# Performance work log

Hardware: AMD Instinct MI355X
Metric: run time of the kernel (lower is better)

Reference implementation:

```python
import jax, jax.numpy as jnp
import numpy as np

LNF, PNF, H = 128, 128, 128
THRESH = 10.0
NORM = 100.0
EPS = 1e-8


def _linear(x, W, b):
    return x @ W + b


def _glorot(key, shape):
    fan_in = shape[0]
    return jax.random.normal(key, shape, dtype=jnp.float32) / jnp.sqrt(jnp.float32(fan_in))


def setup_inputs() -> dict:
    key = jax.random.key(0)
    ks = jax.random.split(key, 20)
    bs, nl, npr = 4, 128, 1024
    inp = {
        "h_ligand": jax.random.normal(ks[0], (bs, nl, LNF), jnp.float32),
        "x_ligand": jax.random.normal(ks[1], (bs, nl, 3), jnp.float32) * 4.0,
        "h_protein": jax.random.normal(ks[2], (bs, npr, PNF), jnp.float32),
        "x_protein": jax.random.normal(ks[3], (bs, npr, 3), jnp.float32) * 4.0,
        "ligand_mask": jnp.ones((bs, nl, 1), jnp.float32),
        "protein_mask": jnp.ones((bs, npr, 1), jnp.float32),
        # attention MLP: (lnf+pnf+1)->H->H->1
        "aW1": _glorot(ks[4], (LNF + PNF + 1, H)), "ab1": jnp.zeros((H,), jnp.float32),
        "aW2": _glorot(ks[5], (H, H)),            "ab2": jnp.zeros((H,), jnp.float32),
        "aW3": _glorot(ks[6], (H, 1)),            "ab3": jnp.zeros((1,), jnp.float32),
        # value MLP: (pnf+1)->H->lnf
        "vW1": _glorot(ks[7], (PNF + 1, H)),      "vb1": jnp.zeros((H,), jnp.float32),
        "vW2": _glorot(ks[8], (H, LNF)),          "vb2": jnp.zeros((LNF,), jnp.float32),
        # coord MLP: (lnf+pnf+1)->H->1
        "cW1": _glorot(ks[9], (LNF + PNF + 1, H)), "cb1": jnp.zeros((H,), jnp.float32),
        "cW2": _glorot(ks[10], (H, 1)),           "cb2": jnp.zeros((1,), jnp.float32),
    }
    return inp


def reference(h_ligand, x_ligand, h_protein, x_protein, ligand_mask, protein_mask,
              aW1, ab1, aW2, ab2, aW3, ab3, vW1, vb1, vW2, vb2, cW1, cb1, cW2, cb2):
    bs, nl, lnf = h_ligand.shape
    npr = h_protein.shape[1]
    # pairwise geometry [bs, nl, np, ...]
    rel = x_ligand[:, :, None, :] - x_protein[:, None, :, :]
    ds = jnp.sum(rel * rel, axis=-1, keepdims=True)           # dist^2
    dist = jnp.sqrt(ds + EPS)
    edge = (dist < THRESH).astype(h_ligand.dtype)             # radius edge mask
    direction = rel / (dist + EPS)
    hl = jnp.broadcast_to(h_ligand[:, :, None, :], (bs, nl, npr, lnf))
    hp = jnp.broadcast_to(h_protein[:, None, :, :], (bs, nl, npr, h_protein.shape[-1]))
    pm = protein_mask[:, None, :, :]                          # [bs,1,np,1]

    pair_in = jnp.concatenate([hl, hp, ds], axis=-1)
    # attention MLP -> sigmoid
    a = jax.nn.silu(_linear(pair_in, aW1, ab1))
    a = jax.nn.silu(_linear(a, aW2, ab2))
    attn = jax.nn.sigmoid(_linear(a, aW3, ab3)) * pm
    # value MLP
    v = jax.nn.silu(_linear(jnp.concatenate([hp, ds], axis=-1), vW1, vb1))
    val = _linear(v, vW2, vb2)
    # feature messages, masked radius aggregation
    h_cross = jnp.sum(attn * val * edge, axis=2) / NORM       # [bs,nl,lnf]
    # coord MLP -> tanh
    c = jax.nn.silu(_linear(pair_in, cW1, cb1))
    cw = jnp.tanh(_linear(c, cW2, cb2)) * pm
    x_cross = jnp.sum(direction * cw * edge, axis=2) / NORM   # [bs,nl,3]

    h_cross = h_cross * ligand_mask
    x_cross = x_cross * ligand_mask
    return h_cross, x_cross
```

## Files before the change

kernel.cpp:

```cpp
#include <hip/hip_runtime.h>
#include <hip/hip_bf16.h>
#include <math.h>

#define HF 128
#define NL 128
#define NP 1024
#define NB 4
#define EPSF 1e-8f

typedef short bf16x8 __attribute__((ext_vector_type(8)));
typedef float f32x4 __attribute__((ext_vector_type(4)));

__device__ __forceinline__ float fast_rcp(float x){ return __builtin_amdgcn_rcpf(x); }
__device__ __forceinline__ float silu_f(float x){ return x*fast_rcp(1.f+__expf(-x)); }
__device__ __forceinline__ float sigmoid_f(float x){ return fast_rcp(1.f+__expf(-x)); }
__device__ __forceinline__ float tanh_f(float x){ return 1.f - 2.f*fast_rcp(1.f+__expf(2.f*x)); }
__device__ __forceinline__ unsigned short f2bf(float f){ __hip_bfloat16 h=__float2bfloat16(f); return *(unsigned short*)&h; }
__device__ __forceinline__ float bf2f(short u){ unsigned int x = ((unsigned int)(unsigned short)u)<<16; float r; __builtin_memcpy(&r,&x,4); return r; }

__global__ __launch_bounds__(128) void precompute_kernel(
    const float* __restrict__ h_ligand, const float* __restrict__ h_protein,
    const float* __restrict__ aW1, const float* __restrict__ ab1,
    const float* __restrict__ vW1, const float* __restrict__ vb1,
    const float* __restrict__ cW1, const float* __restrict__ cb1,
    const float* __restrict__ aW2, const float* __restrict__ vW2,
    float* __restrict__ Al, float* __restrict__ Cl,
    unsigned short* __restrict__ Ap, unsigned short* __restrict__ Vp,
    unsigned short* __restrict__ Cp,
    unsigned short* __restrict__ WaT, unsigned short* __restrict__ WvT)
{
    const int blk = blockIdx.x, n = threadIdx.x;
    if (blk < 64) {
        __shared__ float rows[8][HF];
        const int r0 = blk*8;
        for (int idx=n; idx<8*HF; idx+=128) rows[idx>>7][idx&127] = h_ligand[r0*HF+idx];
        __syncthreads();
        float aA[8], aC[8];
        const float bA = ab1[n], bC = cb1[n];
        #pragma unroll
        for (int r=0;r<8;++r){ aA[r]=bA; aC[r]=bC; }
        #pragma unroll 4
        for (int k=0;k<HF;++k){
            float wA = aW1[k*HF+n], wC = cW1[k*HF+n];
            #pragma unroll
            for (int r=0;r<8;++r){ aA[r]=fmaf(rows[r][k],wA,aA[r]); aC[r]=fmaf(rows[r][k],wC,aC[r]); }
        }
        #pragma unroll
        for (int r=0;r<8;++r){ Al[(r0+r)*HF+n]=aA[r]; Cl[(r0+r)*HF+n]=aC[r]; }
    } else if (blk < 576) {
        __shared__ float rows[8][HF];
        const int r0 = (blk-64)*8;
        for (int idx=n; idx<8*HF; idx+=128) rows[idx>>7][idx&127] = h_protein[r0*HF+idx];
        __syncthreads();
        float aA[8], aV[8], aC[8];
        const float bV = vb1[n];
        #pragma unroll
        for (int r=0;r<8;++r){ aA[r]=0.f; aV[r]=bV; aC[r]=0.f; }
        #pragma unroll 2
        for (int k=0;k<HF;++k){
            float wA = aW1[(HF+k)*HF+n], wV = vW1[k*HF+n], wC = cW1[(HF+k)*HF+n];
            #pragma unroll
            for (int r=0;r<8;++r){
                float h = rows[r][k];
                aA[r]=fmaf(h,wA,aA[r]); aV[r]=fmaf(h,wV,aV[r]); aC[r]=fmaf(h,wC,aC[r]);
            }
        }
        #pragma unroll
        for (int r=0;r<8;++r){
            Ap[(r0+r)*HF+n]=f2bf(aA[r]); Vp[(r0+r)*HF+n]=f2bf(aV[r]); Cp[(r0+r)*HF+n]=f2bf(aC[r]);
        }
    } else {
        const int m = blk - 576;
        const float* W = (m<8) ? aW2 : vW2;
        unsigned short* WT = (m<8) ? WaT : WvT;
        const int n0 = (m&7)*16;
        #pragma unroll
        for (int kb=0; kb<16; ++kb) {
            int k = kb*8 + (n>>4);
            int col = n0 + (n&15);
            WT[col*HF + k] = f2bf(W[k*HF + col]);
        }
    }
}

__global__ __launch_bounds__(256,2) void egnn_main_kernel(
    const float* __restrict__ x_ligand, const float* __restrict__ x_protein,
    const float* __restrict__ ligand_mask, const float* __restrict__ protein_mask,
    const float* __restrict__ aW1, const float* __restrict__ ab2,
    const float* __restrict__ aW3, const float* __restrict__ ab3,
    const float* __restrict__ vW1, const float* __restrict__ vb2,
    const float* __restrict__ cW1, const float* __restrict__ cW2, const float* __restrict__ cb2,
    const float* __restrict__ Al, const float* __restrict__ Cl,
    const unsigned short* __restrict__ Ap, const unsigned short* __restrict__ Vp,
    const unsigned short* __restrict__ Cp,
    const unsigned short* __restrict__ WaT, const unsigned short* __restrict__ WvT,
    float* __restrict__ out)
{
    __shared__ __align__(16) char smem[50176];
    float* ds_all = (float*)(smem + 32768);
    float* pme    = (float*)(smem + 34816);
    float* dirx   = (float*)(smem + 36864);
    float* diry   = (float*)(smem + 38912);
    float* dirz   = (float*)(smem + 40960);
    unsigned short* jlist = (unsigned short*)(smem + 43008);
    float* Al_s   = (float*)(smem + 44032);
    float* Cl_s   = (float*)(smem + 44544);
    float* aw1l   = (float*)(smem + 45056);
    float* cw1l   = (float*)(smem + 45568);
    float* vw1l   = (float*)(smem + 46080);
    float* cW2s   = (float*)(smem + 46592);
    float* attn_part = (float*)(smem + 47104);
    float* attn_e = (float*)(smem + 47360);
    float* hred   = (float*)(smem + 47616);
    float* xw     = (float*)(smem + 48640);
    int* nact_p   = (int*)(smem + 48704);

    const int t = threadIdx.x, lane = t&63, w = t>>6;
    const int wj = w>>1, wn = w&1;
    const int lr = lane&15, lg = lane>>4;
    const int bi = blockIdx.x;
    const int half = bi & 1;
    const int ii = bi >> 1;
    const int b = ii >> 7;
    const int jbase = half*512;

    const float xl0 = x_ligand[ii*3+0], xl1 = x_ligand[ii*3+1], xl2 = x_ligand[ii*3+2];
    const float* xp = x_protein + ((size_t)b*NP + jbase)*3;
    const float* pm = protein_mask + (size_t)b*NP + jbase;
    #pragma unroll
    for (int q=0; q<2; ++q) {
        int jj = q*256 + t;
        float r0 = xl0-xp[jj*3+0], r1 = xl1-xp[jj*3+1], r2 = xl2-xp[jj*3+2];
        float ds = r0*r0+r1*r1+r2*r2;
        float dist = sqrtf(ds+EPSF);
        float inv = fast_rcp(dist+EPSF);
        float e = dist < 10.f ? 1.f : 0.f;
        ds_all[jj]=ds; pme[jj]=pm[jj]*e;
        dirx[jj]=r0*inv; diry[jj]=r1*inv; dirz[jj]=r2*inv;
    }
    if (t < HF) {
        Al_s[t] = Al[(size_t)ii*HF+t];
        Cl_s[t] = Cl[(size_t)ii*HF+t];
        aw1l[t] = aW1[256*HF+t];
        cw1l[t] = cW1[256*HF+t];
        vw1l[t] = vW1[128*HF+t];
        cW2s[t] = cW2[t];
    }
    float ab2v[4], aw3v[4], vb2v[4];
    #pragma unroll
    for (int nt=0; nt<4; ++nt) {
        int n = wn*64 + nt*16 + lr;
        ab2v[nt] = ab2[n]; aw3v[nt] = aW3[n]; vb2v[nt] = vb2[n];
    }
    const float ab3v = ab3[0], cb2v = cb2[0];

    for (int c = t; c < 2048; c += 256) {
        int n = c >> 4, kc = c & 15;
        *(bf16x8*)(smem + n*256 + ((kc*16) ^ ((n&7)<<4))) = *(const bf16x8*)(WaT + n*HF + kc*8);
    }
    __syncthreads();

    if (w == 0) {
        int base = 0;
        for (int c=0; c<8; ++c) {
            int jj = c*64 + lane;
            bool act = pme[jj] > 0.f;
            unsigned long long m = __ballot(act);
            int pos = base + __popcll(m & ((1ull<<lane)-1ull));
            if (act) jlist[pos] = (unsigned short)jj;
            base += __popcll(m);
        }
        if (lane == 0) *nact_p = base;
    }
    bf16x8 wa[4][4], wv[4][4];
    #pragma unroll
    for (int nt = 0; nt < 4; ++nt) {
        int ncol = wn*64 + nt*16 + lr;
        int rb = ncol*256, sw = (ncol & 7) << 4;
        #pragma unroll
        for (int ks = 0; ks < 4; ++ks)
            wa[nt][ks] = *(bf16x8*)(smem + rb + ((lg*16 + ks*64) ^ sw));
    }
    __syncthreads();

    for (int c = t; c < 2048; c += 256) {
        int n = c >> 4, kc = c & 15;
        *(bf16x8*)(smem + n*256 + ((kc*16) ^ ((n&7)<<4))) = *(const bf16x8*)(WvT + n*HF + kc*8);
    }
    __syncthreads();
    #pragma unroll
    for (int nt = 0; nt < 4; ++nt) {
        int ncol = wn*64 + nt*16 + lr;
        int rb = ncol*256, sw = (ncol & 7) << 4;
        #pragma unroll
        for (int ks = 0; ks < 4; ++ks)
            wv[nt][ks] = *(bf16x8*)(smem + rb + ((lg*16 + ks*64) ^ sw));
    }
    __syncthreads();

    const int nact = *nact_p;
    const int ntiles = (nact + 31) >> 5;

    const unsigned short* Ap_b = Ap + ((size_t)b*NP + jbase)*HF;
    const unsigned short* Vp_b = Vp + ((size_t)b*NP + jbase)*HF;
    const unsigned short* Cp_b = Cp + ((size_t)b*NP + jbase)*HF;

    float hacc[4] = {0.f,0.f,0.f,0.f};
    float sae = 0.f;
    float xa0 = 0.f, xa1 = 0.f, xa2 = 0.f;
    const int brow = t >> 4, bcol = (t & 15)*8;
    const int crow = t >> 3, cg = t & 7;

    for (int tile = 0; tile < ntiles; ++tile) {
        const int j0 = tile*32;

        #pragma unroll
        for (int m = 0; m < 2; ++m) {
            const int row = m*16 + brow;
            const int grow = j0 + row;
            const int jl = jlist[grow < nact ? grow : 0];
            const float dsv = ds_all[jl];
            bf16x8 ap = *(const bf16x8*)(Ap_b + (size_t)jl*HF + bcol);
            f32x4 al0 = *(const f32x4*)&Al_s[bcol];
            f32x4 al1 = *(const f32x4*)&Al_s[bcol+4];
            f32x4 w0  = *(const f32x4*)&aw1l[bcol];
            f32x4 w1  = *(const f32x4*)&aw1l[bcol+4];
            bf16x8 pk;
            #pragma unroll
            for (int q = 0; q < 4; ++q) {
                pk[q]   = (short)f2bf(silu_f(al0[q] + bf2f(ap[q])   + dsv*w0[q]));
                pk[q+4] = (short)f2bf(silu_f(al1[q] + bf2f(ap[q+4]) + dsv*w1[q]));
            }
            *(bf16x8*)(smem + row*256 + ((bcol*2) ^ ((row & 7) << 4))) = pk;
        }
        __syncthreads();

        bf16x8 af[4];
        {
            int arow = wj*16 + lr;
            int rb = arow*256, sw = (arow & 7) << 4;
            #pragma unroll
            for (int ks = 0; ks < 4; ++ks)
                af[ks] = *(bf16x8*)(smem + rb + ((lg*16 + ks*64) ^ sw));
        }
        f32x4 acc[4];
        #pragma unroll
        for (int nt = 0; nt < 4; ++nt) {
            acc[nt] = (f32x4){0.f,0.f,0.f,0.f};
            #pragma unroll
            for (int ks = 0; ks < 4; ++ks)
                acc[nt] = __builtin_amdgcn_mfma_f32_16x16x32_bf16(af[ks], wa[nt][ks], acc[nt], 0,0,0);
        }
        {
            const int growc = j0 + crow;
            const bool okc = growc < nact;
            const int jlc = jlist[okc ? growc : 0];
            const float pmec = okc ? pme[jlc] : 0.f;
            const float dsc = ds_all[jlc];
            float part = 0.f;
            const unsigned short* cp = Cp_b + (size_t)jlc*HF + cg*16;
            #pragma unroll
            for (int u = 0; u < 2; ++u) {
                const int ch = cg*16 + u*8;
                bf16x8 cv = *(const bf16x8*)(cp + u*8);
                f32x4 cl0 = *(const f32x4*)&Cl_s[ch];
                f32x4 cl1 = *(const f32x4*)&Cl_s[ch+4];
                f32x4 w0  = *(const f32x4*)&cw1l[ch];
                f32x4 w1  = *(const f32x4*)&cw1l[ch+4];
                f32x4 s0  = *(const f32x4*)&cW2s[ch];
                f32x4 s1  = *(const f32x4*)&cW2s[ch+4];
                #pragma unroll
                for (int q = 0; q < 4; ++q) {
                    part += silu_f(cl0[q] + bf2f(cv[q])   + dsc*w0[q]) * s0[q];
                    part += silu_f(cl1[q] + bf2f(cv[q+4]) + dsc*w1[q]) * s1[q];
                }
            }
            part += __shfl_xor(part,1); part += __shfl_xor(part,2); part += __shfl_xor(part,4);
            if (cg == 0) {
                float cw = tanh_f(part + cb2v) * pmec;
                xa0 = fmaf(dirx[jlc], cw, xa0);
                xa1 = fmaf(diry[jlc], cw, xa1);
                xa2 = fmaf(dirz[jlc], cw, xa2);
            }
        }
        #pragma unroll
        for (int r = 0; r < 4; ++r) {
            float p = 0.f;
            #pragma unroll
            for (int nt = 0; nt < 4; ++nt)
                p += silu_f(acc[nt][r] + ab2v[nt]) * aw3v[nt];
            p += __shfl_xor(p,1); p += __shfl_xor(p,2);
            p += __shfl_xor(p,4); p += __shfl_xor(p,8);
            if (lr == 0) attn_part[wn*32 + wj*16 + lg*4 + r] = p;
        }
        __syncthreads();

        if (t < 32) {
            const int grow = j0 + t;
            const bool ok = grow < nact;
            const int j = jlist[ok ? grow : 0];
            attn_e[t] = sigmoid_f(attn_part[t] + attn_part[32+t] + ab3v) * (ok ? pme[j] : 0.f);
        }
        #pragma unroll
        for (int m = 0; m < 2; ++m) {
            const int row = m*16 + brow;
            const int grow = j0 + row;
            const int jl = jlist[grow < nact ? grow : 0];
            const float dsv = ds_all[jl];
            bf16x8 vp = *(const bf16x8*)(Vp_b + (size_t)jl*HF + bcol);
            f32x4 w0 = *(const f32x4*)&vw1l[bcol];
            f32x4 w1 = *(const f32x4*)&vw1l[bcol+4];
            bf16x8 pk;
            #pragma unroll
            for (int q = 0; q < 4; ++q) {
                pk[q]   = (short)f2bf(silu_f(bf2f(vp[q])   + dsv*w0[q]));
                pk[q+4] = (short)f2bf(silu_f(bf2f(vp[q+4]) + dsv*w1[q]));
            }
            *(bf16x8*)(smem + 8192 + row*256 + ((bcol*2) ^ ((row & 7) << 4))) = pk;
        }
        __syncthreads();

        bf16x8 vf[4];
        {
            int arow = wj*16 + lr;
            int rb = 8192 + arow*256, sw = (arow & 7) << 4;
            #pragma unroll
            for (int ks = 0; ks < 4; ++ks)
                vf[ks] = *(bf16x8*)(smem + rb + ((lg*16 + ks*64) ^ sw));
        }
        float ae[4];
        #pragma unroll
        for (int r = 0; r < 4; ++r) { ae[r] = attn_e[wj*16 + lg*4 + r]; sae += ae[r]; }
        #pragma unroll
        for (int nt = 0; nt < 4; ++nt) {
            f32x4 a = (f32x4){0.f,0.f,0.f,0.f};
            #pragma unroll
            for (int ks = 0; ks < 4; ++ks)
                a = __builtin_amdgcn_mfma_f32_16x16x32_bf16(vf[ks], wv[nt][ks], a, 0,0,0);
            hacc[nt] += ae[0]*a[0] + ae[1]*a[1] + ae[2]*a[2] + ae[3]*a[3];
        }
    }

    #pragma unroll
    for (int nt = 0; nt < 4; ++nt) {
        hacc[nt] += __shfl_xor(hacc[nt],16);
        hacc[nt] += __shfl_xor(hacc[nt],32);
    }
    sae += __shfl_xor(sae,16);
    sae += __shfl_xor(sae,32);
    if (lg == 0) {
        #pragma unroll
        for (int nt = 0; nt < 4; ++nt)
            hred[wj*128 + wn*64 + nt*16 + lr] = hacc[nt] + vb2v[nt]*sae;
    }
    xa0 += __shfl_xor(xa0,1);  xa1 += __shfl_xor(xa1,1);  xa2 += __shfl_xor(xa2,1);
    xa0 += __shfl_xor(xa0,2);  xa1 += __shfl_xor(xa1,2);  xa2 += __shfl_xor(xa2,2);
    xa0 += __shfl_xor(xa0,4);  xa1 += __shfl_xor(xa1,4);  xa2 += __shfl_xor(xa2,4);
    xa0 += __shfl_xor(xa0,8);  xa1 += __shfl_xor(xa1,8);  xa2 += __shfl_xor(xa2,8);
    xa0 += __shfl_xor(xa0,16); xa1 += __shfl_xor(xa1,16); xa2 += __shfl_xor(xa2,16);
    xa0 += __shfl_xor(xa0,32); xa1 += __shfl_xor(xa1,32); xa2 += __shfl_xor(xa2,32);
    if (lane == 0) { xw[w*3+0]=xa0; xw[w*3+1]=xa1; xw[w*3+2]=xa2; }
    __syncthreads();

    const float lm = ligand_mask[ii];
    if (t < HF) {
        float v = (hred[t] + hred[128+t]) * 0.01f * lm;
        atomicAdd(&out[(size_t)ii*HF + t], v);
    }
    if (t < 3) {
        float v = (xw[t] + xw[3+t] + xw[6+t] + xw[9+t]) * 0.01f * lm;
        atomicAdd(&out[(size_t)NB*NL*HF + ii*3 + t], v);
    }
}

extern "C" void kernel_launch(void* const* d_in, const int* in_sizes, int n_in,
                              void* d_out, int out_size, void* d_ws, size_t ws_size,
                              hipStream_t stream) {
    const float* h_ligand     = (const float*)d_in[0];
    const float* x_ligand     = (const float*)d_in[1];
    const float* h_protein    = (const float*)d_in[2];
    const float* x_protein    = (const float*)d_in[3];
    const float* ligand_mask  = (const float*)d_in[4];
    const float* protein_mask = (const float*)d_in[5];
    const float* aW1 = (const float*)d_in[6];
    const float* ab1 = (const float*)d_in[7];
    const float* aW2 = (const float*)d_in[8];
    const float* ab2 = (const float*)d_in[9];
    const float* aW3 = (const float*)d_in[10];
    const float* ab3 = (const float*)d_in[11];
    const float* vW1 = (const float*)d_in[12];
    const float* vb1 = (const float*)d_in[13];
    const float* vW2 = (const float*)d_in[14];
    const float* vb2 = (const float*)d_in[15];
    const float* cW1 = (const float*)d_in[16];
    const float* cb1 = (const float*)d_in[17];
    const float* cW2 = (const float*)d_in[18];
    const float* cb2 = (const float*)d_in[19];

    float* Al = (float*)d_ws;
    float* Cl = Al + 512*HF;
    unsigned short* Ap  = (unsigned short*)(Cl + 512*HF);
    unsigned short* Vp  = Ap + (size_t)NB*NP*HF;
    unsigned short* Cp  = Vp + (size_t)NB*NP*HF;
    unsigned short* WaT = Cp + (size_t)NB*NP*HF;
    unsigned short* WvT = WaT + HF*HF;

    hipMemsetAsync(d_out, 0, (size_t)out_size*sizeof(float), stream);

    precompute_kernel<<<592, 128, 0, stream>>>(
        h_ligand, h_protein, aW1, ab1, vW1, vb1, cW1, cb1, aW2, vW2,
        Al, Cl, Ap, Vp, Cp, WaT, WvT);

    egnn_main_kernel<<<NB*NL*2, 256, 0, stream>>>(
        x_ligand, x_protein, ligand_mask, protein_mask,
        aW1, ab2, aW3, ab3, vW1, vb2, cW1, cW2, cb2,
        Al, Cl, Ap, Vp, Cp, WaT, WvT, (float*)d_out);
}
```

Before: 248.1 us.

## Process 64 protein rows per tile with padded LDS vectors and packed bf16 stores

Doubles the pair tile from 32 to 64 active protein rows, so each wave runs two MFMA row-blocks per stage and the per-tile barrier cost is spread over twice the work. The per-ligand vectors in LDS are padded, every 8 or 16 floats, to avoid bank conflicts on vector reads, and the bf16 conversions now use paired pack intrinsics. The coord MLP uses 4 lanes per row instead of 8, with a shorter shuffle reduction. In exchange it adds an extra barrier per tile, raises register pressure, and wastes more padded work on the last partial tile.

```diff
diff --git a/kernel.cpp b/kernel.cpp
--- a/kernel.cpp
+++ b/kernel.cpp
@@ -17,6 +17,10 @@
 __device__ __forceinline__ float tanh_f(float x){ return 1.f - 2.f*fast_rcp(1.f+__expf(2.f*x)); }
 __device__ __forceinline__ unsigned short f2bf(float f){ __hip_bfloat16 h=__float2bfloat16(f); return *(unsigned short*)&h; }
 __device__ __forceinline__ float bf2f(short u){ unsigned int x = ((unsigned int)(unsigned short)u)<<16; float r; __builtin_memcpy(&r,&x,4); return r; }
+__device__ __forceinline__ unsigned pk2(float a, float b){
+    __hip_bfloat162 h = __float22bfloat162_rn(make_float2(a,b));
+    return *reinterpret_cast<unsigned*>(&h);
+}
 
 __global__ __launch_bounds__(128) void precompute_kernel(
     const float* __restrict__ h_ligand, const float* __restrict__ h_protein,
@@ -96,24 +100,24 @@
     const unsigned short* __restrict__ WaT, const unsigned short* __restrict__ WvT,
     float* __restrict__ out)
 {
-    __shared__ __align__(16) char smem[50176];
+    __shared__ __align__(16) char smem[50432];
     float* ds_all = (float*)(smem + 32768);
     float* pme    = (float*)(smem + 34816);
     float* dirx   = (float*)(smem + 36864);
     float* diry   = (float*)(smem + 38912);
     float* dirz   = (float*)(smem + 40960);
     unsigned short* jlist = (unsigned short*)(smem + 43008);
-    float* Al_s   = (float*)(smem + 44032);
-    float* Cl_s   = (float*)(smem + 44544);
-    float* aw1l   = (float*)(smem + 45056);
-    float* cw1l   = (float*)(smem + 45568);
-    float* vw1l   = (float*)(smem + 46080);
-    float* cW2s   = (float*)(smem + 46592);
-    float* attn_part = (float*)(smem + 47104);
-    float* attn_e = (float*)(smem + 47360);
-    float* hred   = (float*)(smem + 47616);
-    float* xw     = (float*)(smem + 48640);
-    int* nact_p   = (int*)(smem + 48704);
+    float* AlP    = (float*)(smem + 44032);
+    float* aw1P   = (float*)(smem + 44800);
+    float* vw1P   = (float*)(smem + 45568);
+    float* ClP    = (float*)(smem + 46336);
+    float* cw1P   = (float*)(smem + 46976);
+    float* cW2P   = (float*)(smem + 47616);
+    float* attn_part = (float*)(smem + 48256);
+    float* attn_e = (float*)(smem + 48768);
+    float* hred   = (float*)(smem + 49024);
+    float* xw     = (float*)(smem + 50048);
+    int* nact_p   = (int*)(smem + 50096);
 
     const int t = threadIdx.x, lane = t&63, w = t>>6;
     const int wj = w>>1, wn = w&1;
@@ -139,12 +143,14 @@
         dirx[jj]=r0*inv; diry[jj]=r1*inv; dirz[jj]=r2*inv;
     }
     if (t < HF) {
-        Al_s[t] = Al[(size_t)ii*HF+t];
-        Cl_s[t] = Cl[(size_t)ii*HF+t];
-        aw1l[t] = aW1[256*HF+t];
-        cw1l[t] = cW1[256*HF+t];
-        vw1l[t] = vW1[128*HF+t];
-        cW2s[t] = cW2[t];
+        const int iA = t + ((t>>3)<<2);
+        AlP[iA]  = Al[(size_t)ii*HF+t];
+        aw1P[iA] = aW1[256*HF+t];
+        vw1P[iA] = vW1[128*HF+t];
+        const int iC = t + ((t>>4)<<2);
+        ClP[iC]  = Cl[(size_t)ii*HF+t];
+        cw1P[iC] = cW1[256*HF+t];
+        cW2P[iC] = cW2[t];
     }
     float ab2v[4], aw3v[4], vb2v[4];
     #pragma unroll
@@ -182,7 +188,6 @@
             wa[nt][ks] = *(bf16x8*)(smem + rb + ((lg*16 + ks*64) ^ sw));
     }
     __syncthreads();
-
     for (int c = t; c < 2048; c += 256) {
         int n = c >> 4, kc = c & 15;
         *(bf16x8*)(smem + n*256 + ((kc*16) ^ ((n&7)<<4))) = *(const bf16x8*)(WvT + n*HF + kc*8);
@@ -199,57 +204,73 @@
     __syncthreads();
 
     const int nact = *nact_p;
-    const int ntiles = (nact + 31) >> 5;
-
-    const unsigned short* Ap_b = Ap + ((size_t)b*NP + jbase)*HF;
-    const unsigned short* Vp_b = Vp + ((size_t)b*NP + jbase)*HF;
-    const unsigned short* Cp_b = Cp + ((size_t)b*NP + jbase)*HF;
+    const int ntiles = (nact + 63) >> 6;
+
+    const char* ApB = (const char*)(Ap + ((size_t)b*NP + jbase)*HF);
+    const char* VpB = (const char*)(Vp + ((size_t)b*NP + jbase)*HF);
+    const char* CpB = (const char*)(Cp + ((size_t)b*NP + jbase)*HF);
 
     float hacc[4] = {0.f,0.f,0.f,0.f};
     float sae = 0.f;
     float xa0 = 0.f, xa1 = 0.f, xa2 = 0.f;
-    const int brow = t >> 4, bcol = (t & 15)*8;
-    const int crow = t >> 3, cg = t & 7;
+    const int brow = t >> 4;
+    const int bcol2 = (t & 15)*16;
+    const int gbA = (t & 15)*12;
+    const int crow = t >> 2, cg4 = t & 3;
 
     for (int tile = 0; tile < ntiles; ++tile) {
-        const int j0 = tile*32;
-
-        #pragma unroll
-        for (int m = 0; m < 2; ++m) {
+        const int j0 = tile*64;
+
+        #pragma unroll
+        for (int m = 0; m < 4; ++m) {
             const int row = m*16 + brow;
             const int grow = j0 + row;
             const int jl = jlist[grow < nact ? grow : 0];
             const float dsv = ds_all[jl];
-            bf16x8 ap = *(const bf16x8*)(Ap_b + (size_t)jl*HF + bcol);
-            f32x4 al0 = *(const f32x4*)&Al_s[bcol];
-            f32x4 al1 = *(const f32x4*)&Al_s[bcol+4];
-            f32x4 w0  = *(const f32x4*)&aw1l[bcol];
-            f32x4 w1  = *(const f32x4*)&aw1l[bcol+4];
-            bf16x8 pk;
+            bf16x8 ap = *(const bf16x8*)(ApB + jl*256 + bcol2);
+            f32x4 al0 = *(const f32x4*)&AlP[gbA];
+            f32x4 al1 = *(const f32x4*)&AlP[gbA+4];
+            f32x4 w0  = *(const f32x4*)&aw1P[gbA];
+            f32x4 w1  = *(const f32x4*)&aw1P[gbA+4];
+            float f[8];
             #pragma unroll
             for (int q = 0; q < 4; ++q) {
-                pk[q]   = (short)f2bf(silu_f(al0[q] + bf2f(ap[q])   + dsv*w0[q]));
-                pk[q+4] = (short)f2bf(silu_f(al1[q] + bf2f(ap[q+4]) + dsv*w1[q]));
-            }
-            *(bf16x8*)(smem + row*256 + ((bcol*2) ^ ((row & 7) << 4))) = pk;
-        }
-        __syncthreads();
-
-        bf16x8 af[4];
-        {
-            int arow = wj*16 + lr;
-            int rb = arow*256, sw = (arow & 7) << 4;
-            #pragma unroll
-            for (int ks = 0; ks < 4; ++ks)
-                af[ks] = *(bf16x8*)(smem + rb + ((lg*16 + ks*64) ^ sw));
-        }
-        f32x4 acc[4];
-        #pragma unroll
-        for (int nt = 0; nt < 4; ++nt) {
-            acc[nt] = (f32x4){0.f,0.f,0.f,0.f};
-            #pragma unroll
-            for (int ks = 0; ks < 4; ++ks)
-                acc[nt] = __builtin_amdgcn_mfma_f32_16x16x32_bf16(af[ks], wa[nt][ks], acc[nt], 0,0,0);
+                f[q]   = silu_f(al0[q] + bf2f(ap[q])   + dsv*w0[q]);
+                f[q+4] = silu_f(al1[q] + bf2f(ap[q+4]) + dsv*w1[q]);
+            }
+            uint4 pk = { pk2(f[0],f[1]), pk2(f[2],f[3]), pk2(f[4],f[5]), pk2(f[6],f[7]) };
+            *(uint4*)(smem + row*256 + (bcol2 ^ ((row & 7) << 4))) = pk;
+        }
+        __syncthreads();
+
+        #pragma unroll
+        for (int rb = 0; rb < 2; ++rb) {
+            const int arow = rb*32 + wj*16 + lr;
+            bf16x8 af[4];
+            {
+                int rbase = arow*256, sw = (arow & 7) << 4;
+                #pragma unroll
+                for (int ks = 0; ks < 4; ++ks)
+                    af[ks] = *(bf16x8*)(smem + rbase + ((lg*16 + ks*64) ^ sw));
+            }
+            f32x4 acc[4];
+            #pragma unroll
+            for (int nt = 0; nt < 4; ++nt) {
+                acc[nt] = (f32x4){0.f,0.f,0.f,0.f};
+                #pragma unroll
+                for (int ks = 0; ks < 4; ++ks)
+                    acc[nt] = __builtin_amdgcn_mfma_f32_16x16x32_bf16(af[ks], wa[nt][ks], acc[nt], 0,0,0);
+            }
+            #pragma unroll
+            for (int r = 0; r < 4; ++r) {
+                float p = 0.f;
+                #pragma unroll
+                for (int nt = 0; nt < 4; ++nt)
+                    p += silu_f(acc[nt][r] + ab2v[nt]) * aw3v[nt];
+                p += __shfl_xor(p,1); p += __shfl_xor(p,2);
+                p += __shfl_xor(p,4); p += __shfl_xor(p,8);
+                if (lr == 0) attn_part[wn*64 + rb*32 + wj*16 + lg*4 + r] = p;
+            }
         }
         {
             const int growc = j0 + crow;
@@ -258,87 +279,83 @@
             const float pmec = okc ? pme[jlc] : 0.f;
             const float dsc = ds_all[jlc];
             float part = 0.f;
-            const unsigned short* cp = Cp_b + (size_t)jlc*HF + cg*16;
-            #pragma unroll
-            for (int u = 0; u < 2; ++u) {
-                const int ch = cg*16 + u*8;
-                bf16x8 cv = *(const bf16x8*)(cp + u*8);
-                f32x4 cl0 = *(const f32x4*)&Cl_s[ch];
-                f32x4 cl1 = *(const f32x4*)&Cl_s[ch+4];
-                f32x4 w0  = *(const f32x4*)&cw1l[ch];
-                f32x4 w1  = *(const f32x4*)&cw1l[ch+4];
-                f32x4 s0  = *(const f32x4*)&cW2s[ch];
-                f32x4 s1  = *(const f32x4*)&cW2s[ch+4];
+            const char* cp = CpB + jlc*256 + cg4*64;
+            #pragma unroll
+            for (int u = 0; u < 4; ++u) {
+                const int ch = cg4*32 + u*8;
+                const int gi = ch + ((ch>>4)<<2);
+                bf16x8 cv = *(const bf16x8*)(cp + u*16);
+                f32x4 cl0 = *(const f32x4*)&ClP[gi];
+                f32x4 cl1 = *(const f32x4*)&ClP[gi+4];
+                f32x4 w0  = *(const f32x4*)&cw1P[gi];
+                f32x4 w1  = *(const f32x4*)&cw1P[gi+4];
+                f32x4 s0  = *(const f32x4*)&cW2P[gi];
+                f32x4 s1  = *(const f32x4*)&cW2P[gi+4];
                 #pragma unroll
                 for (int q = 0; q < 4; ++q) {
                     part += silu_f(cl0[q] + bf2f(cv[q])   + dsc*w0[q]) * s0[q];
                     part += silu_f(cl1[q] + bf2f(cv[q+4]) + dsc*w1[q]) * s1[q];
                 }
             }
-            part += __shfl_xor(part,1); part += __shfl_xor(part,2); part += __shfl_xor(part,4);
-            if (cg == 0) {
+            part += __shfl_xor(part,1); part += __shfl_xor(part,2);
+            if (cg4 == 0) {
                 float cw = tanh_f(part + cb2v) * pmec;
                 xa0 = fmaf(dirx[jlc], cw, xa0);
                 xa1 = fmaf(diry[jlc], cw, xa1);
                 xa2 = fmaf(dirz[jlc], cw, xa2);
             }
         }
-        #pragma unroll
-        for (int r = 0; r < 4; ++r) {
-            float p = 0.f;
-            #pragma unroll
-            for (int nt = 0; nt < 4; ++nt)
-                p += silu_f(acc[nt][r] + ab2v[nt]) * aw3v[nt];
-            p += __shfl_xor(p,1); p += __shfl_xor(p,2);
-            p += __shfl_xor(p,4); p += __shfl_xor(p,8);
-            if (lr == 0) attn_part[wn*32 + wj*16 + lg*4 + r] = p;
-        }
-        __syncthreads();
-
-        if (t < 32) {
+        __syncthreads();
+
+        if (t < 64) {
             const int grow = j0 + t;
             const bool ok = grow < nact;
             const int j = jlist[ok ? grow : 0];
-            attn_e[t] = sigmoid_f(attn_part[t] + attn_part[32+t] + ab3v) * (ok ? pme[j] : 0.f);
-        }
-        #pragma unroll
-        for (int m = 0; m < 2; ++m) {
+            attn_e[t] = sigmoid_f(attn_part[t] + attn_part[64+t] + ab3v) * (ok ? pme[j] : 0.f);
+        }
+        #pragma unroll
+        for (int m = 0; m < 4; ++m) {
             const int row = m*16 + brow;
             const int grow = j0 + row;
             const int jl = jlist[grow < nact ? grow : 0];
             const float dsv = ds_all[jl];
-            bf16x8 vp = *(const bf16x8*)(Vp_b + (size_t)jl*HF + bcol);
-            f32x4 w0 = *(const f32x4*)&vw1l[bcol];
-            f32x4 w1 = *(const f32x4*)&vw1l[bcol+4];
-            bf16x8 pk;
+            bf16x8 vp = *(const bf16x8*)(VpB + jl*256 + bcol2);
+            f32x4 w0 = *(const f32x4*)&vw1P[gbA];
+            f32x4 w1 = *(const f32x4*)&vw1P[gbA+4];
+            float f[8];
             #pragma unroll
             for (int q = 0; q < 4; ++q) {
-                pk[q]   = (short)f2bf(silu_f(bf2f(vp[q])   + dsv*w0[q]));
-                pk[q+4] = (short)f2bf(silu_f(bf2f(vp[q+4]) + dsv*w1[q]));
-            }
-            *(bf16x8*)(smem + 8192 + row*256 + ((bcol*2) ^ ((row & 7) << 4))) = pk;
-        }
-        __syncthreads();
-
-        bf16x8 vf[4];
-        {
-            int arow = wj*16 + lr;
-            int rb = 8192 + arow*256, sw = (arow & 7) << 4;
-            #pragma unroll
-            for (int ks = 0; ks < 4; ++ks)
-                vf[ks] = *(bf16x8*)(smem + rb + ((lg*16 + ks*64) ^ sw));
-        }
-        float ae[4];
-        #pragma unroll
-        for (int r = 0; r < 4; ++r) { ae[r] = attn_e[wj*16 + lg*4 + r]; sae += ae[r]; }
-        #pragma unroll
-        for (int nt = 0; nt < 4; ++nt) {
-            f32x4 a = (f32x4){0.f,0.f,0.f,0.f};
-            #pragma unroll
-            for (int ks = 0; ks < 4; ++ks)
-                a = __builtin_amdgcn_mfma_f32_16x16x32_bf16(vf[ks], wv[nt][ks], a, 0,0,0);
-            hacc[nt] += ae[0]*a[0] + ae[1]*a[1] + ae[2]*a[2] + ae[3]*a[3];
-        }
+                f[q]   = silu_f(bf2f(vp[q])   + dsv*w0[q]);
+                f[q+4] = silu_f(bf2f(vp[q+4]) + dsv*w1[q]);
+            }
+            uint4 pk = { pk2(f[0],f[1]), pk2(f[2],f[3]), pk2(f[4],f[5]), pk2(f[6],f[7]) };
+            *(uint4*)(smem + 16384 + row*256 + (bcol2 ^ ((row & 7) << 4))) = pk;
+        }
+        __syncthreads();
+
+        #pragma unroll
+        for (int rb = 0; rb < 2; ++rb) {
+            const int arow = rb*32 + wj*16 + lr;
+            bf16x8 vf[4];
+            {
+                int rbase = 16384 + arow*256, sw = (arow & 7) << 4;
+                #pragma unroll
+                for (int ks = 0; ks < 4; ++ks)
+                    vf[ks] = *(bf16x8*)(smem + rbase + ((lg*16 + ks*64) ^ sw));
+            }
+            float ae[4];
+            #pragma unroll
+            for (int r = 0; r < 4; ++r) { ae[r] = attn_e[rb*32 + wj*16 + lg*4 + r]; sae += ae[r]; }
+            #pragma unroll
+            for (int nt = 0; nt < 4; ++nt) {
+                f32x4 a = (f32x4){0.f,0.f,0.f,0.f};
+                #pragma unroll
+                for (int ks = 0; ks < 4; ++ks)
+                    a = __builtin_amdgcn_mfma_f32_16x16x32_bf16(vf[ks], wv[nt][ks], a, 0,0,0);
+                hacc[nt] += ae[0]*a[0] + ae[1]*a[1] + ae[2]*a[2] + ae[3]*a[3];
+            }
+        }
+        __syncthreads();
     }
 
     #pragma unroll
```

Result: no change. 247.6 us (-0.2%).
